# Optimization experiments

Hardware: AMD Instinct MI355X
Metric: run time of the kernel (lower is better)

## Reference

```python
import jax, jax.numpy as jnp
import numpy as np

C = 512
C8 = C // 8

def conv1x1(x, W, b):
    # x: [B,C,H,W], W: [O,C], b: [O] -> [B,O,H,W]
    return jnp.einsum('bchw,oc->bohw', x, W) + b[None, :, None, None]

def setup_inputs() -> dict:
    key = jax.random.key(0)
    ks = jax.random.split(key, 9)
    B, H, Wd = 2, 64, 64
    s = 1.0 / np.sqrt(C)
    return {
        'x1': jax.random.normal(ks[0], (B, C, H, Wd), jnp.float32),
        'x2': jax.random.normal(ks[1], (B, C, H, Wd), jnp.float32),
        'Wb': jax.random.uniform(ks[2], (C8, C), jnp.float32, -s, s),
        'bb': jax.random.uniform(ks[3], (C8,), jnp.float32, -s, s),
        'Wc': jax.random.uniform(ks[4], (C8, C), jnp.float32, -s, s),
        'bc': jax.random.uniform(ks[5], (C8,), jnp.float32, -s, s),
        'Wdd': jax.random.uniform(ks[6], (C, C), jnp.float32, -s, s),
        'bd': jax.random.uniform(ks[7], (C,), jnp.float32, -s, s),
        'alpha': jnp.ones((1,), jnp.float32),
        'beta': jnp.ones((1,), jnp.float32),
    }

def reference(x1, x2, Wb, bb, Wc, bc, Wdd, bd, alpha, beta):
    B, Cc, H, Wsp = x1.shape
    N = H * Wsp
    # projections, flattened to [B, ch, N]
    a1 = conv1x1(x1, Wb, bb).reshape(B, C8, N)   # conv_b(x1)
    b2 = conv1x1(x2, Wc, bc).reshape(B, C8, N)   # conv_c(x2)
    a2 = conv1x1(x2, Wb, bb).reshape(B, C8, N)   # conv_b(x2)
    b1 = conv1x1(x1, Wc, bc).reshape(B, C8, N)   # conv_c(x1)
    f1 = conv1x1(x1, Wdd, bd).reshape(B, Cc, N)  # conv_d(x1)
    f2 = conv1x1(x2, Wdd, bd).reshape(B, Cc, N)  # conv_d(x2)
    # attention_12 = softmax(a1^T @ b2), rows over query positions
    att12 = jax.nn.softmax(jnp.einsum('bcn,bcm->bnm', a1, b2), axis=-1)
    att21 = jax.nn.softmax(jnp.einsum('bcn,bcm->bnm', a2, b1), axis=-1)
    att = jnp.abs(att12 - att21)                 # [B,N,N]
    # feat @ att^T : out[b,c,n] = sum_m f[b,c,m] * att[b,n,m]
    o1 = jnp.einsum('bcm,bnm->bcn', f1, att).reshape(B, Cc, H, Wsp)
    o2 = jnp.einsum('bcm,bnm->bcn', f2, att).reshape(B, Cc, H, Wsp)
    return alpha[0] * o1 + beta[0] * o2
```

## Files before the change

kernel.cpp:

```cpp
#include <hip/hip_runtime.h>
#include <math.h>

#define NB 2
#define CDIM 512
#define NT 4096
#define LOG2E 1.44269504088896f
#define SHIFT 20.0f

typedef unsigned short u16;
typedef __attribute__((ext_vector_type(8))) short short8;
typedef __attribute__((ext_vector_type(4))) float f32x4;

union U8 { u16 v[8]; uint4 u4; };
union U4 { u16 v[4]; uint2 u2; };

__device__ __forceinline__ u16 f2bf(float f) {
    union { float f; unsigned u; } v; v.f = f;
    unsigned r = (v.u + 0x7fffu + ((v.u >> 16) & 1u)) >> 16;
    return (u16)r;
}
__device__ __forceinline__ float bf2f(u16 b) {
    union { float f; unsigned u; } v; v.u = ((unsigned)b) << 16; return v.f;
}
__device__ __forceinline__ float fexp2(float x) {
#if __has_builtin(__builtin_amdgcn_exp2f)
    return __builtin_amdgcn_exp2f(x);
#else
    return exp2f(x);
#endif
}
__device__ __forceinline__ float flog2(float x) {
#if __has_builtin(__builtin_amdgcn_logf)
    return __builtin_amdgcn_logf(x);
#else
    return log2f(x);
#endif
}

__global__ __launch_bounds__(256) void k_convW(
    const float* __restrict__ Wb, const float* __restrict__ Wc, const float* __restrict__ Wd,
    const float* __restrict__ alpha, const float* __restrict__ beta,
    u16* __restrict__ W1, u16* __restrict__ W2f)
{
    int r = blockIdx.x, t = threadIdx.x;
    const float* src; float scale; u16* dst;
    if (r < 640) {
        dst = W1 + (size_t)r * CDIM;
        if (r < 64)       { src = Wb + (size_t)r * CDIM;        scale = LOG2E; }
        else if (r < 128) { src = Wc + (size_t)(r - 64) * CDIM; scale = 1.f; }
        else              { src = Wd + (size_t)(r - 128) * CDIM; scale = alpha[0]; }
    } else {
        int rr = r - 640;
        dst = W2f + (size_t)rr * CDIM;
        src = Wd + (size_t)rr * CDIM;
        scale = beta[0];
    }
    float2 v = *(const float2*)&src[t * 2];
    unsigned p = (unsigned)f2bf(v.x * scale) | ((unsigned)f2bf(v.y * scale) << 16);
    *(unsigned*)&dst[t * 2] = p;
}

__global__ __launch_bounds__(256) void k_prep(
    const float* __restrict__ x1, const float* __restrict__ x2,
    u16* __restrict__ x1T, u16* __restrict__ x2T)
{
    __shared__ float Lt[64][65];
    int t = threadIdx.x;
    int c0 = blockIdx.x * 64, n0 = blockIdx.y * 64;
    int which = blockIdx.z & 1, batch = blockIdx.z >> 1;
    const float* src = (which ? x2 : x1) + (size_t)batch * CDIM * NT;
    u16* dst = (which ? x2T : x1T) + (size_t)batch * NT * CDIM;
    #pragma unroll
    for (int p = 0; p < 4; p++) {
        int cr = p * 16 + (t >> 4), nc = (t & 15) * 4;
        float4 v = *(const float4*)&src[(size_t)(c0 + cr) * NT + n0 + nc];
        Lt[cr][nc] = v.x; Lt[cr][nc + 1] = v.y; Lt[cr][nc + 2] = v.z; Lt[cr][nc + 3] = v.w;
    }
    __syncthreads();
    #pragma unroll
    for (int p = 0; p < 2; p++) {
        int nr = p * 32 + (t >> 3), cc = (t & 7) * 8;
        U8 u;
        #pragma unroll
        for (int j = 0; j < 8; j++) u.v[j] = f2bf(Lt[cc + j][nr]);
        *(uint4*)&dst[(size_t)(n0 + nr) * CDIM + c0 + cc] = u.u4;
    }
}

template<int WHICH>
__global__ __launch_bounds__(256, 2) void k_gemm(
    const u16* __restrict__ W1, const u16* __restrict__ W2f,
    const u16* __restrict__ xT,
    const float* __restrict__ bb, const float* __restrict__ bc, const float* __restrict__ bd,
    const float* __restrict__ alpha, const float* __restrict__ beta,
    u16* __restrict__ yab, u16* __restrict__ ft)
{
    __shared__ u16 Wt[128][72];
    __shared__ u16 Xt[128][72];
    int t = threadIdx.x, lane = t & 63, w = t >> 6, q = lane >> 4, l15 = lane & 15;
    int nT_ = blockIdx.x, oT = blockIdx.y, batch = blockIdx.z;
    int n0 = nT_ * 128, o0 = oT * 128;
    const u16* Wsrc = (WHICH == 1 || oT == 0) ? (W1 + (size_t)o0 * CDIM)
                                              : (W2f + (size_t)(o0 - 128) * CDIM);
    const u16* xb = xT + ((size_t)batch * NT + n0) * CDIM;
    f32x4 acc[2][8];
    #pragma unroll
    for (int a = 0; a < 2; a++)
        #pragma unroll
        for (int b = 0; b < 8; b++) { f32x4 z = {0.f,0.f,0.f,0.f}; acc[a][b] = z; }

    for (int k0 = 0; k0 < CDIM; k0 += 64) {
        if (k0) __syncthreads();
        int r = t >> 1, h = t & 1;
        #pragma unroll
        for (int u = 0; u < 4; u++) {
            *(uint4*)&Wt[r][h * 32 + u * 8] = *(const uint4*)&Wsrc[(size_t)r * CDIM + k0 + h * 32 + u * 8];
            *(uint4*)&Xt[r][h * 32 + u * 8] = *(const uint4*)&xb[(size_t)r * CDIM + k0 + h * 32 + u * 8];
        }
        __syncthreads();
        if (oT == 0) {
            short8 af[2][2];
            #pragma unroll
            for (int ot = 0; ot < 2; ot++)
                #pragma unroll
                for (int kk = 0; kk < 2; kk++)
                    af[ot][kk] = *(const short8*)&Wt[w * 32 + ot * 16 + l15][kk * 32 + q * 8];
            #pragma unroll
            for (int kk = 0; kk < 2; kk++)
                #pragma unroll
                for (int i = 0; i < 8; i++) {
                    short8 bf = *(const short8*)&Xt[i * 16 + l15][kk * 32 + q * 8];
                    #pragma unroll
                    for (int ot = 0; ot < 2; ot++)
                        acc[ot][i] = __builtin_amdgcn_mfma_f32_16x16x32_bf16(af[ot][kk], bf, acc[ot][i], 0, 0, 0);
                }
        } else {
            short8 wf[2][2];
            #pragma unroll
            for (int ct = 0; ct < 2; ct++)
                #pragma unroll
                for (int kk = 0; kk < 2; kk++)
                    wf[ct][kk] = *(const short8*)&Wt[w * 32 + ct * 16 + l15][kk * 32 + q * 8];
            #pragma unroll
            for (int kk = 0; kk < 2; kk++)
                #pragma unroll
                for (int i = 0; i < 8; i++) {
                    short8 xf = *(const short8*)&Xt[i * 16 + l15][kk * 32 + q * 8];
                    #pragma unroll
                    for (int ct = 0; ct < 2; ct++)
                        acc[ct][i] = __builtin_amdgcn_mfma_f32_16x16x32_bf16(xf, wf[ct][kk], acc[ct][i], 0, 0, 0);
                }
        }
    }

    if (oT == 0) {
        #pragma unroll
        for (int ot = 0; ot < 2; ot++)
            #pragma unroll
            for (int i = 0; i < 8; i++) {
                int obase = w * 32 + ot * 16 + q * 4;
                int n = n0 + i * 16 + l15;
                U4 u;
                #pragma unroll
                for (int r = 0; r < 4; r++) {
                    int o = obase + r;
                    float bias = (o < 64) ? bb[o] * LOG2E : bc[o - 64];
                    u.v[r] = f2bf(acc[ot][i][r] + bias);
                }
                *(uint2*)&yab[((size_t)batch * NT + n) * 128 + obase] = u.u2;
            }
    } else {
        float bscale = (WHICH == 2) ? (alpha[0] + beta[0]) : 0.f;
        #pragma unroll
        for (int ct = 0; ct < 2; ct++)
            #pragma unroll
            for (int i = 0; i < 8; i++) {
                int c = (o0 - 128) + w * 32 + ct * 16 + l15;
                int mb = n0 + i * 16 + q * 4;
                u16* dst = &ft[((size_t)batch * CDIM + c) * NT + mb];
                U4 u;
                if (WHICH == 1) {
                    #pragma unroll
                    for (int r = 0; r < 4; r++) u.v[r] = f2bf(acc[ct][i][r]);
                } else {
                    U4 old; old.u2 = *(const uint2*)dst;
                    float bias = bd[c] * bscale;
                    #pragma unroll
                    for (int r = 0; r < 4; r++) u.v[r] = f2bf(acc[ct][i][r] + bf2f(old.v[r]) + bias);
                }
                *(uint2*)dst = u.u2;
            }
    }
}

__global__ __launch_bounds__(256) void k_denom(
    const u16* __restrict__ yab1, const u16* __restrict__ yab2,
    float* __restrict__ denom)
{
    __shared__ u16 a1t[32][72], a2t[32][72];
    __shared__ u16 b1t[128][72], b2t[128][72];
    int t = threadIdx.x, lane = t & 63, w = t >> 6, q = lane >> 4, l15 = lane & 15;
    int x = blockIdx.x & 7;
    int batch = x & 1, mq = x >> 1;
    int n0 = (blockIdx.x >> 3) * 32;
    const u16* y1 = yab1 + (size_t)batch * NT * 128;
    const u16* y2 = yab2 + (size_t)batch * NT * 128;

    *(uint4*)&a1t[t >> 3][(t & 7) * 8] = *(const uint4*)&y1[(size_t)(n0 + (t >> 3)) * 128 + (t & 7) * 8];
    *(uint4*)&a2t[t >> 3][(t & 7) * 8] = *(const uint4*)&y2[(size_t)(n0 + (t >> 3)) * 128 + (t & 7) * 8];
    __syncthreads();

    short8 a1f[2][2], a2f[2][2];
    #pragma unroll
    for (int i = 0; i < 2; i++)
        #pragma unroll
        for (int kk = 0; kk < 2; kk++) {
            a1f[i][kk] = *(const short8*)&a1t[i * 16 + l15][kk * 32 + q * 8];
            a2f[i][kk] = *(const short8*)&a2t[i * 16 + l15][kk * 32 + q * 8];
        }

    float sm[2][2] = {{0.f,0.f},{0.f,0.f}};
    for (int mc = mq * 1024; mc < mq * 1024 + 1024; mc += 128) {
        __syncthreads();
        int r = t >> 1, h = t & 1;
        #pragma unroll
        for (int u = 0; u < 4; u++) {
            *(uint4*)&b1t[r][h * 32 + u * 8] = *(const uint4*)&y1[(size_t)(mc + r) * 128 + 64 + h * 32 + u * 8];
            *(uint4*)&b2t[r][h * 32 + u * 8] = *(const uint4*)&y2[(size_t)(mc + r) * 128 + 64 + h * 32 + u * 8];
        }
        __syncthreads();
        #pragma unroll
        for (int mt = 0; mt < 2; mt++) {
            int ml = w * 32 + mt * 16 + l15;
            short8 bA1k0 = *(const short8*)&b1t[ml][q * 8];
            short8 bA1k1 = *(const short8*)&b1t[ml][32 + q * 8];
            short8 bA2k0 = *(const short8*)&b2t[ml][q * 8];
            short8 bA2k1 = *(const short8*)&b2t[ml][32 + q * 8];
            #pragma unroll
            for (int i = 0; i < 2; i++) {
                f32x4 z = {0.f,0.f,0.f,0.f};
                f32x4 s12 = __builtin_amdgcn_mfma_f32_16x16x32_bf16(bA2k0, a1f[i][0], z, 0, 0, 0);
                s12 = __builtin_amdgcn_mfma_f32_16x16x32_bf16(bA2k1, a1f[i][1], s12, 0, 0, 0);
                f32x4 s21 = __builtin_amdgcn_mfma_f32_16x16x32_bf16(bA1k0, a2f[i][0], z, 0, 0, 0);
                s21 = __builtin_amdgcn_mfma_f32_16x16x32_bf16(bA1k1, a2f[i][1], s21, 0, 0, 0);
                #pragma unroll
                for (int r2 = 0; r2 < 4; r2++) {
                    sm[0][i] += fexp2(s12[r2] - SHIFT);
                    sm[1][i] += fexp2(s21[r2] - SHIFT);
                }
            }
        }
    }
    #pragma unroll
    for (int d = 0; d < 2; d++)
        #pragma unroll
        for (int i = 0; i < 2; i++) {
            float v = sm[d][i];
            v += __shfl_xor(v, 16);
            v += __shfl_xor(v, 32);
            if (q == 0)
                atomicAdd(&denom[((size_t)d * NB + batch) * NT + n0 + i * 16 + l15], v);
        }
}

__global__ __launch_bounds__(256, 2) void k_papply(
    const u16* __restrict__ yab1, const u16* __restrict__ yab2,
    const u16* __restrict__ ft, const float* __restrict__ denom,
    float* __restrict__ out, float* __restrict__ partial)
{
    __shared__ u16 a1t[32][72], a2t[32][72];
    __shared__ u16 b1t[128][72], b2t[128][72];
    __shared__ u16 Pt[32][136];
    int t = threadIdx.x, lane = t & 63, w = t >> 6, q = lane >> 4, l15 = lane & 15;
    int x = blockIdx.x & 7;
    int batch = x & 1, mh = (x >> 1) & 1, nlow = x >> 2;
    int n0 = ((blockIdx.x >> 3) * 2 + nlow) * 32;
    const u16* y1 = yab1 + (size_t)batch * NT * 128;
    const u16* y2 = yab2 + (size_t)batch * NT * 128;
    const u16* ftb = ft + (size_t)batch * CDIM * NT;

    *(uint4*)&a1t[t >> 3][(t & 7) * 8] = *(const uint4*)&y1[(size_t)(n0 + (t >> 3)) * 128 + (t & 7) * 8];
    *(uint4*)&a2t[t >> 3][(t & 7) * 8] = *(const uint4*)&y2[(size_t)(n0 + (t >> 3)) * 128 + (t & 7) * 8];
    __syncthreads();

    short8 a1f[2][2], a2f[2][2];
    #pragma unroll
    for (int i = 0; i < 2; i++)
        #pragma unroll
        for (int kk = 0; kk < 2; kk++) {
            a1f[i][kk] = *(const short8*)&a1t[i * 16 + l15][kk * 32 + q * 8];
            a2f[i][kk] = *(const short8*)&a2t[i * 16 + l15][kk * 32 + q * 8];
        }
    float ls12[2], ls21[2];
    #pragma unroll
    for (int i = 0; i < 2; i++) {
        ls12[i] = SHIFT + flog2(denom[(size_t)batch * NT + n0 + i * 16 + l15]);
        ls21[i] = SHIFT + flog2(denom[((size_t)NB + batch) * NT + n0 + i * 16 + l15]);
    }

    f32x4 o[2][8];
    #pragma unroll
    for (int i = 0; i < 2; i++)
        #pragma unroll
        for (int j = 0; j < 8; j++) { f32x4 z = {0.f,0.f,0.f,0.f}; o[i][j] = z; }

    for (int mc = mh * 2048; mc < mh * 2048 + 2048; mc += 128) {
        __syncthreads();
        int r = t >> 1, h = t & 1;
        #pragma unroll
        for (int u = 0; u < 4; u++) {
            *(uint4*)&b1t[r][h * 32 + u * 8] = *(const uint4*)&y1[(size_t)(mc + r) * 128 + 64 + h * 32 + u * 8];
            *(uint4*)&b2t[r][h * 32 + u * 8] = *(const uint4*)&y2[(size_t)(mc + r) * 128 + 64 + h * 32 + u * 8];
        }
        __syncthreads();
        #pragma unroll
        for (int mt = 0; mt < 2; mt++) {
            int ml = w * 32 + mt * 16 + l15;
            short8 bA1k0 = *(const short8*)&b1t[ml][q * 8];
            short8 bA1k1 = *(const short8*)&b1t[ml][32 + q * 8];
            short8 bA2k0 = *(const short8*)&b2t[ml][q * 8];
            short8 bA2k1 = *(const short8*)&b2t[ml][32 + q * 8];
            #pragma unroll
            for (int i = 0; i < 2; i++) {
                f32x4 z = {0.f,0.f,0.f,0.f};
                f32x4 s12 = __builtin_amdgcn_mfma_f32_16x16x32_bf16(bA2k0, a1f[i][0], z, 0, 0, 0);
                s12 = __builtin_amdgcn_mfma_f32_16x16x32_bf16(bA2k1, a1f[i][1], s12, 0, 0, 0);
                f32x4 s21 = __builtin_amdgcn_mfma_f32_16x16x32_bf16(bA1k0, a2f[i][0], z, 0, 0, 0);
                s21 = __builtin_amdgcn_mfma_f32_16x16x32_bf16(bA1k1, a2f[i][1], s21, 0, 0, 0);
                U4 u;
                #pragma unroll
                for (int r2 = 0; r2 < 4; r2++) {
                    float p12 = fexp2(s12[r2] - ls12[i]);
                    float p21 = fexp2(s21[r2] - ls21[i]);
                    u.v[r2] = f2bf(fabsf(p12 - p21));
                }
                *(uint2*)&Pt[i * 16 + l15][w * 32 + mt * 16 + q * 4] = u.u2;
            }
        }
        __syncthreads();
        short8 pa[2][4];
        #pragma unroll
        for (int i = 0; i < 2; i++)
            #pragma unroll
            for (int kk = 0; kk < 4; kk++)
                pa[i][kk] = *(const short8*)&Pt[i * 16 + l15][kk * 32 + q * 8];
        #pragma unroll
        for (int j = 0; j < 8; j++) {
            const u16* fr = ftb + (size_t)(w * 128 + j * 16 + l15) * NT + mc + q * 8;
            short8 fb0 = *(const short8*)(fr);
            short8 fb1 = *(const short8*)(fr + 32);
            short8 fb2 = *(const short8*)(fr + 64);
            short8 fb3 = *(const short8*)(fr + 96);
            #pragma unroll
            for (int i = 0; i < 2; i++) {
                o[i][j] = __builtin_amdgcn_mfma_f32_16x16x32_bf16(pa[i][0], fb0, o[i][j], 0, 0, 0);
                o[i][j] = __builtin_amdgcn_mfma_f32_16x16x32_bf16(pa[i][1], fb1, o[i][j], 0, 0, 0);
                o[i][j] = __builtin_amdgcn_mfma_f32_16x16x32_bf16(pa[i][2], fb2, o[i][j], 0, 0, 0);
                o[i][j] = __builtin_amdgcn_mfma_f32_16x16x32_bf16(pa[i][3], fb3, o[i][j], 0, 0, 0);
            }
        }
    }

    float* dst = mh ? partial : out;
    #pragma unroll
    for (int i = 0; i < 2; i++)
        #pragma unroll
        for (int j = 0; j < 8; j++) {
            int c = w * 128 + j * 16 + l15;
            *(f32x4*)&dst[((size_t)batch * CDIM + c) * NT + n0 + i * 16 + q * 4] = o[i][j];
        }
}

__global__ __launch_bounds__(256) void k_reduce(
    float* __restrict__ out, const float* __restrict__ part, int n4)
{
    int i = blockIdx.x * 256 + threadIdx.x, stride = gridDim.x * 256;
    float4* o4 = (float4*)out;
    const float4* p4 = (const float4*)part;
    for (int j = i; j < n4; j += stride) {
        float4 a = o4[j], b = p4[j];
        o4[j] = make_float4(a.x + b.x, a.y + b.y, a.z + b.z, a.w + b.w);
    }
}

extern "C" void kernel_launch(void* const* d_in, const int* in_sizes, int n_in,
                              void* d_out, int out_size, void* d_ws, size_t ws_size,
                              hipStream_t stream)
{
    const float* x1 = (const float*)d_in[0];
    const float* x2 = (const float*)d_in[1];
    const float* Wb = (const float*)d_in[2];
    const float* bb = (const float*)d_in[3];
    const float* Wc = (const float*)d_in[4];
    const float* bc = (const float*)d_in[5];
    const float* Wd = (const float*)d_in[6];
    const float* bd = (const float*)d_in[7];
    const float* alpha = (const float*)d_in[8];
    const float* beta  = (const float*)d_in[9];
    float* out = (float*)d_out;

    u16* ws  = (u16*)d_ws;
    u16* x1T = ws;
    u16* x2T = ws + 4194304;
    u16* yab1 = ws + 8388608;
    u16* yab2 = ws + 9437184;
    u16* ft   = ws + 10485760;
    u16* W1   = ws + 14680064;
    u16* W2f  = ws + 15007744;
    float* denom = (float*)(ws + 15269888);
    float* partial = (float*)ws;

    hipMemsetAsync(denom, 0, (size_t)2 * NB * NT * sizeof(float), stream);
    k_convW<<<1152, 256, 0, stream>>>(Wb, Wc, Wd, alpha, beta, W1, W2f);
    k_prep<<<dim3(8, 64, 4), 256, 0, stream>>>(x1, x2, x1T, x2T);
    k_gemm<1><<<dim3(32, 5, 2), 256, 0, stream>>>(W1, W2f, x1T, bb, bc, bd, alpha, beta, yab1, ft);
    k_gemm<2><<<dim3(32, 5, 2), 256, 0, stream>>>(W1, W2f, x2T, bb, bc, bd, alpha, beta, yab2, ft);
    k_denom<<<1024, 256, 0, stream>>>(yab1, yab2, denom);
    k_papply<<<512, 256, 0, stream>>>(yab1, yab2, ft, denom, out, partial);
    k_reduce<<<2048, 256, 0, stream>>>(out, partial, NB * CDIM * NT / 4);
}
```

Measured before the change: 325.2 us.

## Shrink attention tiles, drop LDS staging, and replace reduce kernel with atomics

```diff
diff --git a/kernel.cpp b/kernel.cpp
--- a/kernel.cpp
+++ b/kernel.cpp
@@ -193,61 +193,46 @@
     }
 }
 
-__global__ __launch_bounds__(256) void k_denom(
+__global__ __launch_bounds__(256, 4) void k_denom(
     const u16* __restrict__ yab1, const u16* __restrict__ yab2,
     float* __restrict__ denom)
 {
-    __shared__ u16 a1t[32][72], a2t[32][72];
-    __shared__ u16 b1t[128][72], b2t[128][72];
     int t = threadIdx.x, lane = t & 63, w = t >> 6, q = lane >> 4, l15 = lane & 15;
-    int x = blockIdx.x & 7;
-    int batch = x & 1, mq = x >> 1;
-    int n0 = (blockIdx.x >> 3) * 32;
+    int x = blockIdx.x & 15;
+    int batch = x & 1, m8 = x >> 1;
+    int n0 = (blockIdx.x >> 4) * 32;
     const u16* y1 = yab1 + (size_t)batch * NT * 128;
     const u16* y2 = yab2 + (size_t)batch * NT * 128;
 
-    *(uint4*)&a1t[t >> 3][(t & 7) * 8] = *(const uint4*)&y1[(size_t)(n0 + (t >> 3)) * 128 + (t & 7) * 8];
-    *(uint4*)&a2t[t >> 3][(t & 7) * 8] = *(const uint4*)&y2[(size_t)(n0 + (t >> 3)) * 128 + (t & 7) * 8];
-    __syncthreads();
-
     short8 a1f[2][2], a2f[2][2];
     #pragma unroll
     for (int i = 0; i < 2; i++)
         #pragma unroll
         for (int kk = 0; kk < 2; kk++) {
-            a1f[i][kk] = *(const short8*)&a1t[i * 16 + l15][kk * 32 + q * 8];
-            a2f[i][kk] = *(const short8*)&a2t[i * 16 + l15][kk * 32 + q * 8];
+            a1f[i][kk] = *(const short8*)&y1[(size_t)(n0 + i * 16 + l15) * 128 + kk * 32 + q * 8];
+            a2f[i][kk] = *(const short8*)&y2[(size_t)(n0 + i * 16 + l15) * 128 + kk * 32 + q * 8];
         }
 
     float sm[2][2] = {{0.f,0.f},{0.f,0.f}};
-    for (int mc = mq * 1024; mc < mq * 1024 + 1024; mc += 128) {
-        __syncthreads();
-        int r = t >> 1, h = t & 1;
-        #pragma unroll
-        for (int u = 0; u < 4; u++) {
-            *(uint4*)&b1t[r][h * 32 + u * 8] = *(const uint4*)&y1[(size_t)(mc + r) * 128 + 64 + h * 32 + u * 8];
-            *(uint4*)&b2t[r][h * 32 + u * 8] = *(const uint4*)&y2[(size_t)(mc + r) * 128 + 64 + h * 32 + u * 8];
-        }
-        __syncthreads();
-        #pragma unroll
-        for (int mt = 0; mt < 2; mt++) {
-            int ml = w * 32 + mt * 16 + l15;
-            short8 bA1k0 = *(const short8*)&b1t[ml][q * 8];
-            short8 bA1k1 = *(const short8*)&b1t[ml][32 + q * 8];
-            short8 bA2k0 = *(const short8*)&b2t[ml][q * 8];
-            short8 bA2k1 = *(const short8*)&b2t[ml][32 + q * 8];
-            #pragma unroll
-            for (int i = 0; i < 2; i++) {
-                f32x4 z = {0.f,0.f,0.f,0.f};
-                f32x4 s12 = __builtin_amdgcn_mfma_f32_16x16x32_bf16(bA2k0, a1f[i][0], z, 0, 0, 0);
-                s12 = __builtin_amdgcn_mfma_f32_16x16x32_bf16(bA2k1, a1f[i][1], s12, 0, 0, 0);
-                f32x4 s21 = __builtin_amdgcn_mfma_f32_16x16x32_bf16(bA1k0, a2f[i][0], z, 0, 0, 0);
-                s21 = __builtin_amdgcn_mfma_f32_16x16x32_bf16(bA1k1, a2f[i][1], s21, 0, 0, 0);
-                #pragma unroll
-                for (int r2 = 0; r2 < 4; r2++) {
-                    sm[0][i] += fexp2(s12[r2] - SHIFT);
-                    sm[1][i] += fexp2(s21[r2] - SHIFT);
-                }
+    for (int mc = 0; mc < 512; mc += 64) {
+        int mrow = m8 * 512 + mc + w * 16 + l15;
+        const u16* r1 = y1 + (size_t)mrow * 128 + 64;
+        const u16* r2 = y2 + (size_t)mrow * 128 + 64;
+        short8 b1k0 = *(const short8*)(r1 + q * 8);
+        short8 b1k1 = *(const short8*)(r1 + 32 + q * 8);
+        short8 b2k0 = *(const short8*)(r2 + q * 8);
+        short8 b2k1 = *(const short8*)(r2 + 32 + q * 8);
+        #pragma unroll
+        for (int i = 0; i < 2; i++) {
+            f32x4 z = {0.f,0.f,0.f,0.f};
+            f32x4 s12 = __builtin_amdgcn_mfma_f32_16x16x32_bf16(b2k0, a1f[i][0], z, 0, 0, 0);
+            s12 = __builtin_amdgcn_mfma_f32_16x16x32_bf16(b2k1, a1f[i][1], s12, 0, 0, 0);
+            f32x4 s21 = __builtin_amdgcn_mfma_f32_16x16x32_bf16(b1k0, a2f[i][0], z, 0, 0, 0);
+            s21 = __builtin_amdgcn_mfma_f32_16x16x32_bf16(b1k1, a2f[i][1], s21, 0, 0, 0);
+            #pragma unroll
+            for (int r = 0; r < 4; r++) {
+                sm[0][i] += fexp2(s12[r] - SHIFT);
+                sm[1][i] += fexp2(s21[r] - SHIFT);
             }
         }
     }
@@ -263,123 +248,90 @@
         }
 }
 
-__global__ __launch_bounds__(256, 2) void k_papply(
+__global__ __launch_bounds__(256, 4) void k_papply(
     const u16* __restrict__ yab1, const u16* __restrict__ yab2,
     const u16* __restrict__ ft, const float* __restrict__ denom,
-    float* __restrict__ out, float* __restrict__ partial)
-{
-    __shared__ u16 a1t[32][72], a2t[32][72];
-    __shared__ u16 b1t[128][72], b2t[128][72];
-    __shared__ u16 Pt[32][136];
+    float* __restrict__ out)
+{
+    __shared__ u16 Pt[2][16][72];
     int t = threadIdx.x, lane = t & 63, w = t >> 6, q = lane >> 4, l15 = lane & 15;
-    int x = blockIdx.x & 7;
-    int batch = x & 1, mh = (x >> 1) & 1, nlow = x >> 2;
-    int n0 = ((blockIdx.x >> 3) * 2 + nlow) * 32;
+    int x = blockIdx.x & 3;
+    int batch = x & 1, mh = x >> 1;
+    int n0 = (blockIdx.x >> 2) * 16;
     const u16* y1 = yab1 + (size_t)batch * NT * 128;
     const u16* y2 = yab2 + (size_t)batch * NT * 128;
     const u16* ftb = ft + (size_t)batch * CDIM * NT;
 
-    *(uint4*)&a1t[t >> 3][(t & 7) * 8] = *(const uint4*)&y1[(size_t)(n0 + (t >> 3)) * 128 + (t & 7) * 8];
-    *(uint4*)&a2t[t >> 3][(t & 7) * 8] = *(const uint4*)&y2[(size_t)(n0 + (t >> 3)) * 128 + (t & 7) * 8];
-    __syncthreads();
-
-    short8 a1f[2][2], a2f[2][2];
-    #pragma unroll
-    for (int i = 0; i < 2; i++)
-        #pragma unroll
-        for (int kk = 0; kk < 2; kk++) {
-            a1f[i][kk] = *(const short8*)&a1t[i * 16 + l15][kk * 32 + q * 8];
-            a2f[i][kk] = *(const short8*)&a2t[i * 16 + l15][kk * 32 + q * 8];
-        }
-    float ls12[2], ls21[2];
-    #pragma unroll
-    for (int i = 0; i < 2; i++) {
-        ls12[i] = SHIFT + flog2(denom[(size_t)batch * NT + n0 + i * 16 + l15]);
-        ls21[i] = SHIFT + flog2(denom[((size_t)NB + batch) * NT + n0 + i * 16 + l15]);
-    }
-
-    f32x4 o[2][8];
-    #pragma unroll
-    for (int i = 0; i < 2; i++)
-        #pragma unroll
-        for (int j = 0; j < 8; j++) { f32x4 z = {0.f,0.f,0.f,0.f}; o[i][j] = z; }
-
-    for (int mc = mh * 2048; mc < mh * 2048 + 2048; mc += 128) {
+    short8 a1f[2], a2f[2];
+    #pragma unroll
+    for (int kk = 0; kk < 2; kk++) {
+        a1f[kk] = *(const short8*)&y1[(size_t)(n0 + l15) * 128 + kk * 32 + q * 8];
+        a2f[kk] = *(const short8*)&y2[(size_t)(n0 + l15) * 128 + kk * 32 + q * 8];
+    }
+    float ls12 = SHIFT + flog2(denom[(size_t)batch * NT + n0 + l15]);
+    float ls21 = SHIFT + flog2(denom[((size_t)NB + batch) * NT + n0 + l15]);
+
+    f32x4 o[8];
+    #pragma unroll
+    for (int j = 0; j < 8; j++) { f32x4 z = {0.f,0.f,0.f,0.f}; o[j] = z; }
+
+    int pb = 0;
+    for (int mc = 0; mc < 2048; mc += 64) {
+        int mabs = mh * 2048 + mc;
+        int mrow = mabs + w * 16 + l15;
+        const u16* r1 = y1 + (size_t)mrow * 128 + 64;
+        const u16* r2 = y2 + (size_t)mrow * 128 + 64;
+        short8 b1k0 = *(const short8*)(r1 + q * 8);
+        short8 b1k1 = *(const short8*)(r1 + 32 + q * 8);
+        short8 b2k0 = *(const short8*)(r2 + q * 8);
+        short8 b2k1 = *(const short8*)(r2 + 32 + q * 8);
+        f32x4 z = {0.f,0.f,0.f,0.f};
+        f32x4 s12 = __builtin_amdgcn_mfma_f32_16x16x32_bf16(b2k0, a1f[0], z, 0, 0, 0);
+        s12 = __builtin_amdgcn_mfma_f32_16x16x32_bf16(b2k1, a1f[1], s12, 0, 0, 0);
+        f32x4 s21 = __builtin_amdgcn_mfma_f32_16x16x32_bf16(b1k0, a2f[0], z, 0, 0, 0);
+        s21 = __builtin_amdgcn_mfma_f32_16x16x32_bf16(b1k1, a2f[1], s21, 0, 0, 0);
+        U4 u;
+        #pragma unroll
+        for (int r = 0; r < 4; r++) {
+            float p12 = fexp2(s12[r] - ls12);
+            float p21 = fexp2(s21[r] - ls21);
+            u.v[r] = f2bf(fabsf(p12 - p21));
+        }
+        *(uint2*)&Pt[pb][l15][w * 16 + q * 4] = u.u2;
         __syncthreads();
-        int r = t >> 1, h = t & 1;
-        #pragma unroll
-        for (int u = 0; u < 4; u++) {
-            *(uint4*)&b1t[r][h * 32 + u * 8] = *(const uint4*)&y1[(size_t)(mc + r) * 128 + 64 + h * 32 + u * 8];
-            *(uint4*)&b2t[r][h * 32 + u * 8] = *(const uint4*)&y2[(size_t)(mc + r) * 128 + 64 + h * 32 + u * 8];
-        }
-        __syncthreads();
-        #pragma unroll
-        for (int mt = 0; mt < 2; mt++) {
-            int ml = w * 32 + mt * 16 + l15;
-            short8 bA1k0 = *(const short8*)&b1t[ml][q * 8];
-            short8 bA1k1 = *(const short8*)&b1t[ml][32 + q * 8];
-            short8 bA2k0 = *(const short8*)&b2t[ml][q * 8];
-            short8 bA2k1 = *(const short8*)&b2t[ml][32 + q * 8];
-            #pragma unroll
-            for (int i = 0; i < 2; i++) {
-                f32x4 z = {0.f,0.f,0.f,0.f};
-                f32x4 s12 = __builtin_amdgcn_mfma_f32_16x16x32_bf16(bA2k0, a1f[i][0], z, 0, 0, 0);
-                s12 = __builtin_amdgcn_mfma_f32_16x16x32_bf16(bA2k1, a1f[i][1], s12, 0, 0, 0);
-                f32x4 s21 = __builtin_amdgcn_mfma_f32_16x16x32_bf16(bA1k0, a2f[i][0], z, 0, 0, 0);
-                s21 = __builtin_amdgcn_mfma_f32_16x16x32_bf16(bA1k1, a2f[i][1], s21, 0, 0, 0);
-                U4 u;
-                #pragma unroll
-                for (int r2 = 0; r2 < 4; r2++) {
-                    float p12 = fexp2(s12[r2] - ls12[i]);
-                    float p21 = fexp2(s21[r2] - ls21[i]);
-                    u.v[r2] = f2bf(fabsf(p12 - p21));
-                }
-                *(uint2*)&Pt[i * 16 + l15][w * 32 + mt * 16 + q * 4] = u.u2;
+
+        short8 pa0 = *(const short8*)&Pt[pb][l15][q * 8];
+        short8 pa1 = *(const short8*)&Pt[pb][l15][32 + q * 8];
+
+        const u16* fbase = ftb + mabs;
+        short8 fc0, fc1;
+        {
+            const u16* fr = fbase + (size_t)(w * 128 + l15) * NT;
+            fc0 = *(const short8*)(fr + q * 8);
+            fc1 = *(const short8*)(fr + 32 + q * 8);
+        }
+        #pragma unroll
+        for (int j = 0; j < 8; j++) {
+            short8 fn0, fn1;
+            if (j < 7) {
+                const u16* fr = fbase + (size_t)(w * 128 + (j + 1) * 16 + l15) * NT;
+                fn0 = *(const short8*)(fr + q * 8);
+                fn1 = *(const short8*)(fr + 32 + q * 8);
             }
-        }
-        __syncthreads();
-        short8 pa[2][4];
-        #pragma unroll
-        for (int i = 0; i < 2; i++)
-            #pragma unroll
-            for (int kk = 0; kk < 4; kk++)
-                pa[i][kk] = *(const short8*)&Pt[i * 16 + l15][kk * 32 + q * 8];
-        #pragma unroll
-        for (int j = 0; j < 8; j++) {
-            const u16* fr = ftb + (size_t)(w * 128 + j * 16 + l15) * NT + mc + q * 8;
-            short8 fb0 = *(const short8*)(fr);
-            short8 fb1 = *(const short8*)(fr + 32);
-            short8 fb2 = *(const short8*)(fr + 64);
-            short8 fb3 = *(const short8*)(fr + 96);
-            #pragma unroll
-            for (int i = 0; i < 2; i++) {
-                o[i][j] = __builtin_amdgcn_mfma_f32_16x16x32_bf16(pa[i][0], fb0, o[i][j], 0, 0, 0);
-                o[i][j] = __builtin_amdgcn_mfma_f32_16x16x32_bf16(pa[i][1], fb1, o[i][j], 0, 0, 0);
-                o[i][j] = __builtin_amdgcn_mfma_f32_16x16x32_bf16(pa[i][2], fb2, o[i][j], 0, 0, 0);
-                o[i][j] = __builtin_amdgcn_mfma_f32_16x16x32_bf16(pa[i][3], fb3, o[i][j], 0, 0, 0);
-            }
-        }
-    }
-
-    float* dst = mh ? partial : out;
-    #pragma unroll
-    for (int i = 0; i < 2; i++)
-        #pragma unroll
-        for (int j = 0; j < 8; j++) {
-            int c = w * 128 + j * 16 + l15;
-            *(f32x4*)&dst[((size_t)batch * CDIM + c) * NT + n0 + i * 16 + q * 4] = o[i][j];
-        }
-}
-
-__global__ __launch_bounds__(256) void k_reduce(
-    float* __restrict__ out, const float* __restrict__ part, int n4)
-{
-    int i = blockIdx.x * 256 + threadIdx.x, stride = gridDim.x * 256;
-    float4* o4 = (float4*)out;
-    const float4* p4 = (const float4*)part;
-    for (int j = i; j < n4; j += stride) {
-        float4 a = o4[j], b = p4[j];
-        o4[j] = make_float4(a.x + b.x, a.y + b.y, a.z + b.z, a.w + b.w);
+            o[j] = __builtin_amdgcn_mfma_f32_16x16x32_bf16(pa0, fc0, o[j], 0, 0, 0);
+            o[j] = __builtin_amdgcn_mfma_f32_16x16x32_bf16(pa1, fc1, o[j], 0, 0, 0);
+            if (j < 7) { fc0 = fn0; fc1 = fn1; }
+        }
+        pb ^= 1;
+    }
+
+    #pragma unroll
+    for (int j = 0; j < 8; j++) {
+        int c = w * 128 + j * 16 + l15;
+        float* dst = &out[((size_t)batch * CDIM + c) * NT + n0 + q * 4];
+        #pragma unroll
+        for (int r = 0; r < 4; r++)
+            atomicAdd(dst + r, o[j][r]);
     }
 }
 
@@ -408,14 +360,13 @@
     u16* W1   = ws + 14680064;
     u16* W2f  = ws + 15007744;
     float* denom = (float*)(ws + 15269888);
-    float* partial = (float*)ws;
 
     hipMemsetAsync(denom, 0, (size_t)2 * NB * NT * sizeof(float), stream);
+    hipMemsetAsync(out, 0, (size_t)NB * CDIM * NT * sizeof(float), stream);
     k_convW<<<1152, 256, 0, stream>>>(Wb, Wc, Wd, alpha, beta, W1, W2f);
     k_prep<<<dim3(8, 64, 4), 256, 0, stream>>>(x1, x2, x1T, x2T);
     k_gemm<1><<<dim3(32, 5, 2), 256, 0, stream>>>(W1, W2f, x1T, bb, bc, bd, alpha, beta, yab1, ft);
     k_gemm<2><<<dim3(32, 5, 2), 256, 0, stream>>>(W1, W2f, x2T, bb, bc, bd, alpha, beta, yab2, ft);
-    k_denom<<<1024, 256, 0, stream>>>(yab1, yab2, denom);
-    k_papply<<<512, 256, 0, stream>>>(yab1, yab2, ft, denom, out, partial);
-    k_reduce<<<2048, 256, 0, stream>>>(out, partial, NB * CDIM * NT / 4);
-}
+    k_denom<<<2048, 256, 0, stream>>>(yab1, yab2, denom);
+    k_papply<<<1024, 256, 0, stream>>>(yab1, yab2, ft, denom, out);
+}
```

After: 591.0 us. +81.7%, slower.

## Drop LDS staging in denom, prefetch B tiles and feature fragments in papply

Applied to the files above, without the earlier changes.

```diff
diff --git a/kernel.cpp b/kernel.cpp
--- a/kernel.cpp
+++ b/kernel.cpp
@@ -193,61 +193,46 @@
     }
 }
 
-__global__ __launch_bounds__(256) void k_denom(
+__global__ __launch_bounds__(256, 4) void k_denom(
     const u16* __restrict__ yab1, const u16* __restrict__ yab2,
     float* __restrict__ denom)
 {
-    __shared__ u16 a1t[32][72], a2t[32][72];
-    __shared__ u16 b1t[128][72], b2t[128][72];
     int t = threadIdx.x, lane = t & 63, w = t >> 6, q = lane >> 4, l15 = lane & 15;
-    int x = blockIdx.x & 7;
-    int batch = x & 1, mq = x >> 1;
-    int n0 = (blockIdx.x >> 3) * 32;
+    int x = blockIdx.x & 15;
+    int batch = x & 1, m8 = x >> 1;
+    int n0 = (blockIdx.x >> 4) * 32;
     const u16* y1 = yab1 + (size_t)batch * NT * 128;
     const u16* y2 = yab2 + (size_t)batch * NT * 128;
 
-    *(uint4*)&a1t[t >> 3][(t & 7) * 8] = *(const uint4*)&y1[(size_t)(n0 + (t >> 3)) * 128 + (t & 7) * 8];
-    *(uint4*)&a2t[t >> 3][(t & 7) * 8] = *(const uint4*)&y2[(size_t)(n0 + (t >> 3)) * 128 + (t & 7) * 8];
-    __syncthreads();
-
     short8 a1f[2][2], a2f[2][2];
     #pragma unroll
     for (int i = 0; i < 2; i++)
         #pragma unroll
         for (int kk = 0; kk < 2; kk++) {
-            a1f[i][kk] = *(const short8*)&a1t[i * 16 + l15][kk * 32 + q * 8];
-            a2f[i][kk] = *(const short8*)&a2t[i * 16 + l15][kk * 32 + q * 8];
+            a1f[i][kk] = *(const short8*)&y1[(size_t)(n0 + i * 16 + l15) * 128 + kk * 32 + q * 8];
+            a2f[i][kk] = *(const short8*)&y2[(size_t)(n0 + i * 16 + l15) * 128 + kk * 32 + q * 8];
         }
 
     float sm[2][2] = {{0.f,0.f},{0.f,0.f}};
-    for (int mc = mq * 1024; mc < mq * 1024 + 1024; mc += 128) {
-        __syncthreads();
-        int r = t >> 1, h = t & 1;
-        #pragma unroll
-        for (int u = 0; u < 4; u++) {
-            *(uint4*)&b1t[r][h * 32 + u * 8] = *(const uint4*)&y1[(size_t)(mc + r) * 128 + 64 + h * 32 + u * 8];
-            *(uint4*)&b2t[r][h * 32 + u * 8] = *(const uint4*)&y2[(size_t)(mc + r) * 128 + 64 + h * 32 + u * 8];
-        }
-        __syncthreads();
-        #pragma unroll
-        for (int mt = 0; mt < 2; mt++) {
-            int ml = w * 32 + mt * 16 + l15;
-            short8 bA1k0 = *(const short8*)&b1t[ml][q * 8];
-            short8 bA1k1 = *(const short8*)&b1t[ml][32 + q * 8];
-            short8 bA2k0 = *(const short8*)&b2t[ml][q * 8];
-            short8 bA2k1 = *(const short8*)&b2t[ml][32 + q * 8];
-            #pragma unroll
-            for (int i = 0; i < 2; i++) {
-                f32x4 z = {0.f,0.f,0.f,0.f};
-                f32x4 s12 = __builtin_amdgcn_mfma_f32_16x16x32_bf16(bA2k0, a1f[i][0], z, 0, 0, 0);
-                s12 = __builtin_amdgcn_mfma_f32_16x16x32_bf16(bA2k1, a1f[i][1], s12, 0, 0, 0);
-                f32x4 s21 = __builtin_amdgcn_mfma_f32_16x16x32_bf16(bA1k0, a2f[i][0], z, 0, 0, 0);
-                s21 = __builtin_amdgcn_mfma_f32_16x16x32_bf16(bA1k1, a2f[i][1], s21, 0, 0, 0);
-                #pragma unroll
-                for (int r2 = 0; r2 < 4; r2++) {
-                    sm[0][i] += fexp2(s12[r2] - SHIFT);
-                    sm[1][i] += fexp2(s21[r2] - SHIFT);
-                }
+    for (int mc = 0; mc < 512; mc += 64) {
+        int mrow = m8 * 512 + mc + w * 16 + l15;
+        const u16* r1 = y1 + (size_t)mrow * 128 + 64;
+        const u16* r2 = y2 + (size_t)mrow * 128 + 64;
+        short8 b1k0 = *(const short8*)(r1 + q * 8);
+        short8 b1k1 = *(const short8*)(r1 + 32 + q * 8);
+        short8 b2k0 = *(const short8*)(r2 + q * 8);
+        short8 b2k1 = *(const short8*)(r2 + 32 + q * 8);
+        #pragma unroll
+        for (int i = 0; i < 2; i++) {
+            f32x4 z = {0.f,0.f,0.f,0.f};
+            f32x4 s12 = __builtin_amdgcn_mfma_f32_16x16x32_bf16(b2k0, a1f[i][0], z, 0, 0, 0);
+            s12 = __builtin_amdgcn_mfma_f32_16x16x32_bf16(b2k1, a1f[i][1], s12, 0, 0, 0);
+            f32x4 s21 = __builtin_amdgcn_mfma_f32_16x16x32_bf16(b1k0, a2f[i][0], z, 0, 0, 0);
+            s21 = __builtin_amdgcn_mfma_f32_16x16x32_bf16(b1k1, a2f[i][1], s21, 0, 0, 0);
+            #pragma unroll
+            for (int r = 0; r < 4; r++) {
+                sm[0][i] += fexp2(s12[r] - SHIFT);
+                sm[1][i] += fexp2(s21[r] - SHIFT);
             }
         }
     }
@@ -268,28 +253,24 @@
     const u16* __restrict__ ft, const float* __restrict__ denom,
     float* __restrict__ out, float* __restrict__ partial)
 {
-    __shared__ u16 a1t[32][72], a2t[32][72];
-    __shared__ u16 b1t[128][72], b2t[128][72];
+    __shared__ u16 b1t[128][72];
+    __shared__ u16 b2t[128][72];
     __shared__ u16 Pt[32][136];
     int t = threadIdx.x, lane = t & 63, w = t >> 6, q = lane >> 4, l15 = lane & 15;
-    int x = blockIdx.x & 7;
-    int batch = x & 1, mh = (x >> 1) & 1, nlow = x >> 2;
-    int n0 = ((blockIdx.x >> 3) * 2 + nlow) * 32;
+    int xcd = blockIdx.x & 7;
+    int batch = xcd & 1, mh = (xcd >> 1) & 1, nbit = (xcd >> 2) & 1;
+    int n0 = ((blockIdx.x >> 3) * 2 + nbit) * 32;
     const u16* y1 = yab1 + (size_t)batch * NT * 128;
     const u16* y2 = yab2 + (size_t)batch * NT * 128;
     const u16* ftb = ft + (size_t)batch * CDIM * NT;
 
-    *(uint4*)&a1t[t >> 3][(t & 7) * 8] = *(const uint4*)&y1[(size_t)(n0 + (t >> 3)) * 128 + (t & 7) * 8];
-    *(uint4*)&a2t[t >> 3][(t & 7) * 8] = *(const uint4*)&y2[(size_t)(n0 + (t >> 3)) * 128 + (t & 7) * 8];
-    __syncthreads();
-
     short8 a1f[2][2], a2f[2][2];
     #pragma unroll
     for (int i = 0; i < 2; i++)
         #pragma unroll
         for (int kk = 0; kk < 2; kk++) {
-            a1f[i][kk] = *(const short8*)&a1t[i * 16 + l15][kk * 32 + q * 8];
-            a2f[i][kk] = *(const short8*)&a2t[i * 16 + l15][kk * 32 + q * 8];
+            a1f[i][kk] = *(const short8*)&y1[(size_t)(n0 + i * 16 + l15) * 128 + kk * 32 + q * 8];
+            a2f[i][kk] = *(const short8*)&y2[(size_t)(n0 + i * 16 + l15) * 128 + kk * 32 + q * 8];
         }
     float ls12[2], ls21[2];
     #pragma unroll
@@ -304,15 +285,41 @@
         #pragma unroll
         for (int j = 0; j < 8; j++) { f32x4 z = {0.f,0.f,0.f,0.f}; o[i][j] = z; }
 
-    for (int mc = mh * 2048; mc < mh * 2048 + 2048; mc += 128) {
+    int sr = t >> 1, sh = t & 1;
+    const int mbeg = mh * 2048, mend = mh * 2048 + 2048;
+    uint4 sb1[4], sb2[4];
+    #pragma unroll
+    for (int u = 0; u < 4; u++) {
+        sb1[u] = *(const uint4*)&y1[(size_t)(mbeg + sr) * 128 + 64 + sh * 32 + u * 8];
+        sb2[u] = *(const uint4*)&y2[(size_t)(mbeg + sr) * 128 + 64 + sh * 32 + u * 8];
+    }
+
+    for (int mc = mbeg; mc < mend; mc += 128) {
         __syncthreads();
-        int r = t >> 1, h = t & 1;
         #pragma unroll
         for (int u = 0; u < 4; u++) {
-            *(uint4*)&b1t[r][h * 32 + u * 8] = *(const uint4*)&y1[(size_t)(mc + r) * 128 + 64 + h * 32 + u * 8];
-            *(uint4*)&b2t[r][h * 32 + u * 8] = *(const uint4*)&y2[(size_t)(mc + r) * 128 + 64 + h * 32 + u * 8];
+            *(uint4*)&b1t[sr][sh * 32 + u * 8] = sb1[u];
+            *(uint4*)&b2t[sr][sh * 32 + u * 8] = sb2[u];
         }
         __syncthreads();
+
+        if (mc + 128 < mend) {
+            #pragma unroll
+            for (int u = 0; u < 4; u++) {
+                sb1[u] = *(const uint4*)&y1[(size_t)(mc + 128 + sr) * 128 + 64 + sh * 32 + u * 8];
+                sb2[u] = *(const uint4*)&y2[(size_t)(mc + 128 + sr) * 128 + 64 + sh * 32 + u * 8];
+            }
+        }
+        short8 F[4][4];
+        #pragma unroll
+        for (int jj = 0; jj < 4; jj++) {
+            const u16* fr = ftb + (size_t)(w * 128 + jj * 16 + l15) * NT + mc + q * 8;
+            F[jj][0] = *(const short8*)(fr);
+            F[jj][1] = *(const short8*)(fr + 32);
+            F[jj][2] = *(const short8*)(fr + 64);
+            F[jj][3] = *(const short8*)(fr + 96);
+        }
+
         #pragma unroll
         for (int mt = 0; mt < 2; mt++) {
             int ml = w * 32 + mt * 16 + l15;
@@ -344,13 +351,17 @@
             #pragma unroll
             for (int kk = 0; kk < 4; kk++)
                 pa[i][kk] = *(const short8*)&Pt[i * 16 + l15][kk * 32 + q * 8];
+
         #pragma unroll
         for (int j = 0; j < 8; j++) {
-            const u16* fr = ftb + (size_t)(w * 128 + j * 16 + l15) * NT + mc + q * 8;
-            short8 fb0 = *(const short8*)(fr);
-            short8 fb1 = *(const short8*)(fr + 32);
-            short8 fb2 = *(const short8*)(fr + 64);
-            short8 fb3 = *(const short8*)(fr + 96);
+            short8 fb0 = F[j & 3][0], fb1 = F[j & 3][1], fb2 = F[j & 3][2], fb3 = F[j & 3][3];
+            if (j < 4) {
+                const u16* fr = ftb + (size_t)(w * 128 + (j + 4) * 16 + l15) * NT + mc + q * 8;
+                F[j][0] = *(const short8*)(fr);
+                F[j][1] = *(const short8*)(fr + 32);
+                F[j][2] = *(const short8*)(fr + 64);
+                F[j][3] = *(const short8*)(fr + 96);
+            }
             #pragma unroll
             for (int i = 0; i < 2; i++) {
                 o[i][j] = __builtin_amdgcn_mfma_f32_16x16x32_bf16(pa[i][0], fb0, o[i][j], 0, 0, 0);
@@ -415,7 +426,7 @@
     k_prep<<<dim3(8, 64, 4), 256, 0, stream>>>(x1, x2, x1T, x2T);
     k_gemm<1><<<dim3(32, 5, 2), 256, 0, stream>>>(W1, W2f, x1T, bb, bc, bd, alpha, beta, yab1, ft);
     k_gemm<2><<<dim3(32, 5, 2), 256, 0, stream>>>(W1, W2f, x2T, bb, bc, bd, alpha, beta, yab2, ft);
-    k_denom<<<1024, 256, 0, stream>>>(yab1, yab2, denom);
+    k_denom<<<2048, 256, 0, stream>>>(yab1, yab2, denom);
     k_papply<<<512, 256, 0, stream>>>(yab1, yab2, ft, denom, out, partial);
     k_reduce<<<2048, 256, 0, stream>>>(out, partial, NB * CDIM * NT / 4);
 }
```

Result: slower. 391.4 us (+20.4%).
